# Kernel optimization log

Hardware: AMD Instinct MI355X
Metric: run time of the kernel (lower is better)

The kernel has to match this reference:

```python
import jax, jax.numpy as jnp
import numpy as np

NUM_HEADS = 12
SEQ_H = 32
SEQ_W = 32
D_HALF = 32
ROPE_BASE = 10000.0
LN_EPS = 1e-5


def build_rope_cache(seq_len, head_dim, base=ROPE_BASE):
    inv_freq = 1.0 / base ** (jnp.arange(0, head_dim, 2, dtype=jnp.float32) / head_dim)
    t = jnp.arange(seq_len, dtype=jnp.float32)
    freqs = jnp.outer(t, inv_freq)  # [seq_len, head_dim//2]
    cos = jnp.repeat(jnp.cos(freqs), 2, axis=-1)  # [seq_len, head_dim]
    sin = jnp.repeat(jnp.sin(freqs), 2, axis=-1)
    return cos, sin


def apply_rope(x, cos, sin):
    # x: [B,H,N,d_sub], cos/sin: [N,d_sub]
    x_even, x_odd = x[..., ::2], x[..., 1::2]
    x_rot = jnp.stack([-x_odd, x_even], axis=-1).reshape(x.shape)
    return x * cos[None, None] + x_rot * sin[None, None]


def setup_inputs() -> dict:
    key = jax.random.key(0)
    ks = jax.random.split(key, 3)
    B, N, D = 8, 1025, 768
    return {
        "x": jax.random.normal(ks[0], (B, N, D), dtype=jnp.float32),
        "ln_g": jnp.ones((D,), dtype=jnp.float32),
        "ln_b": jnp.zeros((D,), dtype=jnp.float32),
        "w_qkv": jax.random.normal(ks[1], (3 * D, D), dtype=jnp.float32) * 0.02,
        "w_proj": jax.random.normal(ks[2], (D, D), dtype=jnp.float32) * 0.02,
        "b_proj": jnp.zeros((D,), dtype=jnp.float32),
    }


def reference(x, ln_g, ln_b, w_qkv, w_proj, b_proj):
    B, N, D = x.shape
    H = NUM_HEADS
    hd = D // H
    d2 = D_HALF
    scale = hd ** -0.5

    # LayerNorm
    mu = jnp.mean(x, axis=-1, keepdims=True)
    var = jnp.mean(jnp.square(x - mu), axis=-1, keepdims=True)
    xn = (x - mu) * jax.lax.rsqrt(var + LN_EPS) * ln_g + ln_b

    # QKV projection (no bias)
    qkv = jnp.einsum("bnd,ed->bne", xn, w_qkv).reshape(B, N, 3, H, hd)
    qkv = jnp.transpose(qkv, (2, 0, 3, 1, 4))  # [3,B,H,N,hd]
    q, k, v = qkv[0], qkv[1], qkv[2]

    # 2D position ids (CLS token -> row 0, col 0)
    patch_lin = jnp.arange(N - 1)
    rows = patch_lin // SEQ_W
    cols = patch_lin % SEQ_W
    zero = jnp.zeros((1,), dtype=patch_lin.dtype)
    row_ids = jnp.concatenate([zero, rows])
    col_ids = jnp.concatenate([zero, cols])

    cos_row, sin_row = build_rope_cache(SEQ_H, d2)
    cos_col, sin_col = build_rope_cache(SEQ_W, d2)
    cos_r, sin_r = cos_row[row_ids], sin_row[row_ids]  # [N,d2]
    cos_c, sin_c = cos_col[col_ids], sin_col[col_ids]

    q = jnp.concatenate(
        [apply_rope(q[..., :d2], cos_r, sin_r), apply_rope(q[..., d2:], cos_c, sin_c)], axis=-1)
    k = jnp.concatenate(
        [apply_rope(k[..., :d2], cos_r, sin_r), apply_rope(k[..., d2:], cos_c, sin_c)], axis=-1)

    attn = jnp.einsum("bhqd,bhkd->bhqk", q, k) * scale
    attn = jax.nn.softmax(attn, axis=-1)
    out = jnp.einsum("bhqk,bhkd->bhqd", attn, v)  # [B,H,N,hd]
    out = jnp.transpose(out, (0, 2, 1, 3)).reshape(B, N, D)
    return jnp.einsum("bnd,ed->bne", out, w_proj) + b_proj
```

## Files before the change

kernel.cpp:

```cpp
#include <hip/hip_runtime.h>
#include <hip/hip_bf16.h>

typedef unsigned short u16;

#define B_      8
#define N_      1025
#define D_      768
#define H_      12
#define HD_     64
#define M_REAL  (B_ * N_)
#define M_PAD   8320
#define QKVC    (3 * D_)
#define LN_BLK  (M_REAL / 4)

typedef __attribute__((ext_vector_type(8))) short bf16x8;
typedef __attribute__((ext_vector_type(4))) float f32x4;

static __device__ __forceinline__ float bf2f(u16 u) {
    union { unsigned int i; float f; } v; v.i = ((unsigned int)u) << 16; return v.f;
}
static __device__ __forceinline__ u16 f2bf(float f) {
    union { float f; unsigned int i; } v; v.f = f;
    unsigned int x = v.i;
    return (u16)((x + 0x7fffu + ((x >> 16) & 1u)) >> 16);
}
static __device__ __forceinline__ unsigned int cvtpk(float a, float b) {
    unsigned int r;
    asm volatile("v_cvt_pk_bf16_f32 %0, %1, %2" : "=v"(r) : "v"(a), "v"(b));
    return r;
}

static __device__ __forceinline__ void g2l16(const u16* g, u16* l) {
    __builtin_amdgcn_global_load_lds(
        (const __attribute__((address_space(1))) unsigned int*)g,
        (__attribute__((address_space(3))) unsigned int*)l, 16, 0, 0);
}

__global__ __launch_bounds__(256)
void ln_f2b_kernel(const float* __restrict__ x, const float* __restrict__ g,
                   const float* __restrict__ bvec, u16* __restrict__ xn,
                   const float* __restrict__ wq, u16* __restrict__ wqb,
                   const float* __restrict__ wp, u16* __restrict__ wpb)
{
    const int tid = threadIdx.x;
    if (blockIdx.x >= LN_BLK) {
        int i = (blockIdx.x - LN_BLK) * 1024 + tid * 4;
        const float* src; u16* dst;
        if (i < QKVC * D_) { src = wq + i; dst = wqb + i; }
        else { src = wp + (i - QKVC * D_); dst = wpb + (i - QKVC * D_); }
        float4 v = *(const float4*)src;
        dst[0] = f2bf(v.x); dst[1] = f2bf(v.y);
        dst[2] = f2bf(v.z); dst[3] = f2bf(v.w);
        return;
    }
    const int wave = tid >> 6, lane = tid & 63;
    const int row  = blockIdx.x * 4 + wave;
    const float* xr = x + (size_t)row * D_;
    float4 v[3];
    float s = 0.f, ss = 0.f;
#pragma unroll
    for (int j = 0; j < 3; j++) {
        float4 t = *(const float4*)&xr[j * 256 + lane * 4];
        v[j] = t;
        s  += (t.x + t.y) + (t.z + t.w);
        ss += (t.x * t.x + t.y * t.y) + (t.z * t.z + t.w * t.w);
    }
#pragma unroll
    for (int off = 1; off < 64; off <<= 1) {
        s  += __shfl_xor(s,  off);
        ss += __shfl_xor(ss, off);
    }
    const float mean = s * (1.0f / D_);
    const float var  = ss * (1.0f / D_) - mean * mean;
    const float rs   = rsqrtf(var + 1e-5f);
    u16* outr = xn + (size_t)row * D_;
#pragma unroll
    for (int j = 0; j < 3; j++) {
        int c = j * 256 + lane * 4;
        float4 g4 = *(const float4*)&g[c];
        float4 b4 = *(const float4*)&bvec[c];
        u16 o[4];
        o[0] = f2bf((v[j].x - mean) * rs * g4.x + b4.x);
        o[1] = f2bf((v[j].y - mean) * rs * g4.y + b4.y);
        o[2] = f2bf((v[j].z - mean) * rs * g4.z + b4.z);
        o[3] = f2bf((v[j].w - mean) * rs * g4.w + b4.w);
        *(uint2*)&outr[c] = *(const uint2*)o;
    }
}

template <typename OutT, bool ROPE>
__global__ __launch_bounds__(256)
void gemm_bt(const u16* __restrict__ A, const u16* __restrict__ B,
             OutT* __restrict__ C, const float* __restrict__ bias,
             int M_real, int Ncols, int K,
             int BM, int BN, int gh, int gw, int PC)
{
    const int l   = blockIdx.x;
    const int xcd = l & 7;
    const int i0  = l >> 3;
    const int pr  = xcd / PC, pc = xcd % PC;
    const int bm  = pr * gh + (i0 % gh);
    const int bn  = pc * gw + (i0 / gh);
    if (bm >= BM || bn >= BN) return;

    __shared__ __align__(16) unsigned char smem[34816];
    u16* As0 = (u16*)smem;
    u16* Bs0 = (u16*)(smem + 8192);
    u16*   ep16 = (u16*)smem;
    float* ep32 = (float*)smem;

    const int tid  = threadIdx.x;
    const int wave = tid >> 6, lane = tid & 63;
    const int wm   = (wave >> 1) * 64, wn = (wave & 1) * 64;
    const int lrow = lane & 15, lq = lane >> 4;
    const int lrow4 = lane >> 2, lchunk = lane & 3;

    int ar0 = bm * 128 + wave * 16 + lrow4;       if (ar0 >= M_real) ar0 = M_real - 1;
    int ar1 = bm * 128 + (wave + 4) * 16 + lrow4; if (ar1 >= M_real) ar1 = M_real - 1;
    const u16* apg0 = A + (size_t)ar0 * K + lchunk * 8;
    const u16* apg1 = A + (size_t)ar1 * K + lchunk * 8;
    const u16* bpg0 = B + (size_t)(bn * 128 + wave * 16 + lrow4) * K + lchunk * 8;
    const u16* bpg1 = B + (size_t)(bn * 128 + (wave + 4) * 16 + lrow4) * K + lchunk * 8;
    u16* asl0 = As0 + wave * 512;       u16* asl1 = As0 + (wave + 4) * 512;
    u16* bsl0 = Bs0 + wave * 512;       u16* bsl1 = Bs0 + (wave + 4) * 512;
    const int bufoff = 8192;

    f32x4 acc[4][4];
#pragma unroll
    for (int i = 0; i < 4; i++)
#pragma unroll
        for (int j = 0; j < 4; j++)
            acc[i][j] = (f32x4){0.f, 0.f, 0.f, 0.f};

    g2l16(apg0, asl0); g2l16(apg1, asl1);
    g2l16(bpg0, bsl0); g2l16(bpg1, bsl1);

    const int kTiles = K / 32;
    for (int kt = 0; kt < kTiles; kt++) {
        const int cur = kt & 1;
        if (kt + 1 < kTiles) {
            const int k1 = (kt + 1) * 32;
            const int no = (cur ^ 1) * bufoff;
            g2l16(apg0 + k1, asl0 + no); g2l16(apg1 + k1, asl1 + no);
            g2l16(bpg0 + k1, bsl0 + no); g2l16(bpg1 + k1, bsl1 + no);
            asm volatile("s_waitcnt vmcnt(4)" ::: "memory");
        } else {
            asm volatile("s_waitcnt vmcnt(0)" ::: "memory");
        }
        __builtin_amdgcn_s_barrier();

        const u16* Asr = As0 + cur * bufoff;
        const u16* Bsr = Bs0 + cur * bufoff;
        bf16x8 af[4], bfr[4];
#pragma unroll
        for (int i = 0; i < 4; i++) {
            af[i]  = *(const bf16x8*)&Asr[(wm + i * 16 + lrow) * 32 + lq * 8];
            bfr[i] = *(const bf16x8*)&Bsr[(wn + i * 16 + lrow) * 32 + lq * 8];
        }
        __builtin_amdgcn_s_setprio(1);
#pragma unroll
        for (int i = 0; i < 4; i++)
#pragma unroll
            for (int j = 0; j < 4; j++)
                acc[i][j] = __builtin_amdgcn_mfma_f32_16x16x32_bf16(af[i], bfr[j], acc[i][j], 0, 0, 0);
        __builtin_amdgcn_s_setprio(0);
        __builtin_amdgcn_s_barrier();
    }
    __syncthreads();

    if constexpr (sizeof(OutT) == 2) {
#pragma unroll
        for (int j = 0; j < 4; j++) {
            int gcol = bn * 128 + wn + j * 16 + lrow;
            float bv = bias ? bias[gcol] : 0.f;
            int qk = gcol / D_;
            int dh = gcol & 63;
            int half = dh >> 5, ii = (dh & 31) >> 1;
            float sgn = (dh & 1) ? 1.f : -1.f;
            float invf = exp2f(-(float)ii * 0.8304820237218406f);
#pragma unroll
            for (int i = 0; i < 4; i++)
#pragma unroll
                for (int r = 0; r < 4; r++) {
                    int grow = bm * 128 + wm + i * 16 + lq * 4 + r;
                    float val = acc[i][j][r] + bv;
                    if constexpr (ROPE) {
                        if (qk < 2) {
                            float partner = __shfl_xor(val, 1);
                            int n = grow % N_;
                            int pl = n - 1;
                            int pos = (n == 0) ? 0 : (half ? (pl & 31) : (pl >> 5));
                            float ang = (float)pos * invf;
                            val = val * __cosf(ang) + sgn * partner * __sinf(ang);
                            if (qk == 0) val *= 0.125f;
                        }
                    }
                    ep16[(wm + i * 16 + lq * 4 + r) * 136 + wn + j * 16 + lrow] = f2bf(val);
                }
        }
        __syncthreads();
#pragma unroll
        for (int c = 0; c < 8; c++) {
            int idx = tid + c * 256;
            int row = idx >> 4, l16 = idx & 15;
            int grow = bm * 128 + row;
            if (grow < M_real)
                *(uint4*)((u16*)C + (size_t)grow * Ncols + bn * 128 + l16 * 8) =
                    *(const uint4*)&ep16[row * 136 + l16 * 8];
        }
    } else {
#pragma unroll
        for (int s = 0; s < 2; s++) {
            if (s) __syncthreads();
            if (wm == s * 64) {
#pragma unroll
                for (int j = 0; j < 4; j++) {
                    int gcol = bn * 128 + wn + j * 16 + lrow;
                    float bv = bias ? bias[gcol] : 0.f;
#pragma unroll
                    for (int i = 0; i < 4; i++)
#pragma unroll
                        for (int r = 0; r < 4; r++)
                            ep32[(i * 16 + lq * 4 + r) * 132 + wn + j * 16 + lrow] =
                                acc[i][j][r] + bv;
                }
            }
            __syncthreads();
#pragma unroll
            for (int c = 0; c < 8; c++) {
                int idx = tid + c * 256;
                int row = idx >> 5, l32 = idx & 31;
                int grow = bm * 128 + s * 64 + row;
                if (grow < M_real)
                    *(uint4*)((float*)C + (size_t)grow * Ncols + bn * 128 + l32 * 4) =
                        *(const uint4*)&ep32[row * 132 + l32 * 4];
            }
        }
    }
}

__global__ __launch_bounds__(256)
void attn_mfma(const u16* __restrict__ qkv, u16* __restrict__ out)
{
    __shared__ __align__(16) u16 Kt[2][64][64];
    __shared__ __align__(16) u16 Vt[2][64][64];

    const int l   = blockIdx.x;
    const int xcd = l & 7;
    const int j0  = l >> 3;
    const int bh  = xcd * 12 + j0 / 5;
    const int b  = bh / H_, h = bh % H_;
    const int q0 = (j0 % 5) * 256;
    const int tid  = threadIdx.x;
    const int wave = tid >> 6, lane = tid & 63;
    const int lm = lane & 15, lq = lane >> 4;
    const int qw = q0 + wave * 64;

    const int vcol = (lane & 35) | ((lane & 12) << 1) | ((lane & 16) >> 2);

    bf16x8 qf[4][2];
#pragma unroll
    for (int sq = 0; sq < 4; sq++) {
        int qrow = qw + sq * 16 + lm; if (qrow > N_ - 1) qrow = N_ - 1;
        const u16* qptr = qkv + (size_t)(b * N_ + qrow) * QKVC + h * HD_;
        qf[sq][0] = *(const bf16x8*)(qptr + lq * 8);
        qf[sq][1] = *(const bf16x8*)(qptr + 32 + lq * 8);
    }

    float l_r[4] = {0.f, 0.f, 0.f, 0.f};
    f32x4 o_acc[4][4];
#pragma unroll
    for (int sq = 0; sq < 4; sq++)
#pragma unroll
        for (int t = 0; t < 4; t++)
            o_acc[sq][t] = (f32x4){0.f, 0.f, 0.f, 0.f};

    bf16x8 kreg[2], vreg[2];
    {
        int krow = lane; if (krow > N_ - 1) krow = N_ - 1;
        const u16* kvp = qkv + (size_t)(b * N_ + krow) * QKVC + h * HD_;
#pragma unroll
        for (int p = 0; p < 2; p++) {
            int dg = wave + p * 4;
            kreg[p] = *(const bf16x8*)(kvp + D_ + dg * 8);
            vreg[p] = *(const bf16x8*)(kvp + 2 * D_ + dg * 8);
        }
    }

    const int kTiles = (N_ + 63) / 64;
    for (int kt = 0; kt < kTiles; kt++) {
        const int kbase = kt * 64;
        const int buf = kt & 1;

#pragma unroll
        for (int pp = 0; pp < 2; pp++) {
            int dg = wave + pp * 4;
            *(bf16x8*)&Kt[buf][lane][(dg ^ (lane & 7)) * 8] = kreg[pp];
#pragma unroll
            for (int j = 0; j < 8; j++)
                Vt[buf][dg * 8 + j][vcol ^ (j << 3)] = (u16)vreg[pp][j];
        }

        if (kt + 1 < kTiles) {
            int krow = kbase + 64 + lane; if (krow > N_ - 1) krow = N_ - 1;
            const u16* kvp = qkv + (size_t)(b * N_ + krow) * QKVC + h * HD_;
#pragma unroll
            for (int pp = 0; pp < 2; pp++) {
                int dg = wave + pp * 4;
                kreg[pp] = *(const bf16x8*)(kvp + D_ + dg * 8);
                vreg[pp] = *(const bf16x8*)(kvp + 2 * D_ + dg * 8);
            }
        }

        asm volatile("s_waitcnt lgkmcnt(0)" ::: "memory");
        __builtin_amdgcn_s_barrier();

        f32x4 sc[4][4];
        __builtin_amdgcn_s_setprio(1);
#pragma unroll
        for (int st = 0; st < 4; st++) {
            const int krow = st * 16 + lm;
            const int c0 = lq ^ (krow & 7);
            bf16x8 kf0 = *(const bf16x8*)&Kt[buf][krow][c0 * 8];
            bf16x8 kf1 = *(const bf16x8*)&Kt[buf][krow][(c0 ^ 4) * 8];
#pragma unroll
            for (int sq = 0; sq < 4; sq++) {
                f32x4 s4 = (f32x4){0.f, 0.f, 0.f, 0.f};
                s4 = __builtin_amdgcn_mfma_f32_16x16x32_bf16(kf0, qf[sq][0], s4, 0, 0, 0);
                s4 = __builtin_amdgcn_mfma_f32_16x16x32_bf16(kf1, qf[sq][1], s4, 0, 0, 0);
                sc[sq][st] = s4;
            }
        }
        __builtin_amdgcn_s_setprio(0);

        const bool lastT = (kt == kTiles - 1);
        bf16x8 pa[4][2];
#pragma unroll
        for (int sq = 0; sq < 4; sq++) {
            union { bf16x8 v; unsigned int u[4]; } pk0, pk1;
#pragma unroll
            for (int st = 0; st < 4; st++) {
                float p0 = __expf(sc[sq][st][0]);
                float p1 = __expf(sc[sq][st][1]);
                float p2 = __expf(sc[sq][st][2]);
                float p3 = __expf(sc[sq][st][3]);
                if (lastT) {
                    const int keyb = kbase + st * 16 + lq * 4;
                    if (keyb + 0 >= N_) p0 = 0.f;
                    if (keyb + 1 >= N_) p1 = 0.f;
                    if (keyb + 2 >= N_) p2 = 0.f;
                    if (keyb + 3 >= N_) p3 = 0.f;
                }
                l_r[sq] += (p0 + p1) + (p2 + p3);
                unsigned int lo = cvtpk(p0, p1);
                unsigned int hi = cvtpk(p2, p3);
                if      (st == 0) { pk0.u[0] = lo; pk0.u[1] = hi; }
                else if (st == 1) { pk0.u[2] = lo; pk0.u[3] = hi; }
                else if (st == 2) { pk1.u[0] = lo; pk1.u[1] = hi; }
                else              { pk1.u[2] = lo; pk1.u[3] = hi; }
            }
            pa[sq][0] = pk0.v; pa[sq][1] = pk1.v;
        }

        __builtin_amdgcn_s_setprio(1);
#pragma unroll
        for (int nt = 0; nt < 4; nt++) {
            const int vrow = nt * 16 + lm;
            const int d0 = lq ^ (vrow & 7);
            bf16x8 vb0 = *(const bf16x8*)&Vt[buf][vrow][d0 * 8];
            bf16x8 vb1 = *(const bf16x8*)&Vt[buf][vrow][(d0 ^ 4) * 8];
#pragma unroll
            for (int sq = 0; sq < 4; sq++) {
                o_acc[sq][nt] = __builtin_amdgcn_mfma_f32_16x16x32_bf16(pa[sq][0], vb0, o_acc[sq][nt], 0, 0, 0);
                o_acc[sq][nt] = __builtin_amdgcn_mfma_f32_16x16x32_bf16(pa[sq][1], vb1, o_acc[sq][nt], 0, 0, 0);
            }
        }
        __builtin_amdgcn_s_setprio(0);
    }

    float lfull[4];
#pragma unroll
    for (int sq = 0; sq < 4; sq++) {
        float l2 = l_r[sq];
        l2 += __shfl_xor(l2, 16);
        l2 += __shfl_xor(l2, 32);
        lfull[sq] = l2;
    }

#pragma unroll
    for (int sq = 0; sq < 4; sq++)
#pragma unroll
        for (int r = 0; r < 4; r++) {
            int q = qw + sq * 16 + lq * 4 + r;
            if (q < N_) {
                float inv = 1.0f / __shfl(lfull[sq], lq * 4 + r);
                u16* orow = out + (size_t)(b * N_ + q) * D_ + h * HD_ + lm;
#pragma unroll
                for (int nt = 0; nt < 4; nt++)
                    orow[nt * 16] = f2bf(o_acc[sq][nt][r] * inv);
            }
        }
}

extern "C" void kernel_launch(void* const* d_in, const int* in_sizes, int n_in,
                              void* d_out, int out_size, void* d_ws, size_t ws_size,
                              hipStream_t stream)
{
    const float* x      = (const float*)d_in[0];
    const float* ln_g   = (const float*)d_in[1];
    const float* ln_b   = (const float*)d_in[2];
    const float* w_qkv  = (const float*)d_in[3];
    const float* w_proj = (const float*)d_in[4];
    const float* b_proj = (const float*)d_in[5];

    u16* wqkv_b  = (u16*)d_ws;
    u16* wproj_b = wqkv_b + (size_t)QKVC * D_;
    u16* xn      = wproj_b + (size_t)D_ * D_;
    u16* qkv     = xn + (size_t)M_PAD * D_;
    u16* attno   = xn;

    ln_f2b_kernel<<<LN_BLK + (QKVC * D_ + D_ * D_) / 1024, 256, 0, stream>>>(
        x, ln_g, ln_b, xn, w_qkv, wqkv_b, w_proj, wproj_b);

    gemm_bt<u16, true><<<1224, 256, 0, stream>>>(
        xn, wqkv_b, qkv, nullptr, M_REAL, QKVC, D_,
        65, 18, 17, 9, 2);

    attn_mfma<<<480, 256, 0, stream>>>(qkv, attno);

    gemm_bt<float, false><<<432, 256, 0, stream>>>(
        attno, wproj_b, (float*)d_out, b_proj, M_REAL, D_, D_,
        65, 6, 9, 6, 1);
}
```

Before: 208.1 us.

## Enlarge GEMM block tile to 256x128 with 128x64 per-wave tiles

Both GEMMs now use 256-row by 128-column block tiles instead of 128x128. Each wave computes 8x4 MFMA tiles, and A fragments are loaded inside the loop. The change aims to reuse each loaded B tile across more rows and cut block count and global traffic per FLOP. In exchange it raises accumulator registers and LDS use (48KB), which may lower occupancy, and grid counts drop (648 and 240 blocks), which can underfill the CUs, especially for the output projection. The epilogues are reworked into staged passes to fit the larger tile.

New measurement: 293.2 us. 40.9% more time.

```diff
diff --git a/kernel.cpp b/kernel.cpp
--- a/kernel.cpp
+++ b/kernel.cpp
@@ -103,37 +103,45 @@
     const int bn  = pc * gw + (i0 / gh);
     if (bm >= BM || bn >= BN) return;
 
-    __shared__ __align__(16) unsigned char smem[34816];
+    __shared__ __align__(16) unsigned char smem[49152];
     u16* As0 = (u16*)smem;
-    u16* Bs0 = (u16*)(smem + 8192);
+    u16* Bs0 = (u16*)(smem + 16384);
     u16*   ep16 = (u16*)smem;
     float* ep32 = (float*)smem;
+    const int bufoff = 12288;
 
     const int tid  = threadIdx.x;
     const int wave = tid >> 6, lane = tid & 63;
-    const int wm   = (wave >> 1) * 64, wn = (wave & 1) * 64;
+    const int wr   = wave >> 1, wc = wave & 1;
     const int lrow = lane & 15, lq = lane >> 4;
     const int lrow4 = lane >> 2, lchunk = lane & 3;
 
-    int ar0 = bm * 128 + wave * 16 + lrow4;       if (ar0 >= M_real) ar0 = M_real - 1;
-    int ar1 = bm * 128 + (wave + 4) * 16 + lrow4; if (ar1 >= M_real) ar1 = M_real - 1;
-    const u16* apg0 = A + (size_t)ar0 * K + lchunk * 8;
-    const u16* apg1 = A + (size_t)ar1 * K + lchunk * 8;
-    const u16* bpg0 = B + (size_t)(bn * 128 + wave * 16 + lrow4) * K + lchunk * 8;
-    const u16* bpg1 = B + (size_t)(bn * 128 + (wave + 4) * 16 + lrow4) * K + lchunk * 8;
-    u16* asl0 = As0 + wave * 512;       u16* asl1 = As0 + (wave + 4) * 512;
-    u16* bsl0 = Bs0 + wave * 512;       u16* bsl1 = Bs0 + (wave + 4) * 512;
-    const int bufoff = 8192;
-
-    f32x4 acc[4][4];
-#pragma unroll
-    for (int i = 0; i < 4; i++)
+    const u16* apg[4]; u16* asl[4];
+    const u16* bpg[2]; u16* bsl[2];
+#pragma unroll
+    for (int t = 0; t < 4; t++) {
+        int ar = bm * 256 + wave * 16 + t * 64 + lrow4;
+        if (ar >= M_real) ar = M_real - 1;
+        apg[t] = A + (size_t)ar * K + lchunk * 8;
+        asl[t] = As0 + (wave * 16 + t * 64) * 32;
+    }
+#pragma unroll
+    for (int t = 0; t < 2; t++) {
+        bpg[t] = B + (size_t)(bn * 128 + wave * 16 + t * 64 + lrow4) * K + lchunk * 8;
+        bsl[t] = Bs0 + (wave * 16 + t * 64) * 32;
+    }
+
+    f32x4 acc[8][4];
+#pragma unroll
+    for (int i = 0; i < 8; i++)
 #pragma unroll
         for (int j = 0; j < 4; j++)
             acc[i][j] = (f32x4){0.f, 0.f, 0.f, 0.f};
 
-    g2l16(apg0, asl0); g2l16(apg1, asl1);
-    g2l16(bpg0, bsl0); g2l16(bpg1, bsl1);
+#pragma unroll
+    for (int t = 0; t < 4; t++) g2l16(apg[t], asl[t]);
+#pragma unroll
+    for (int t = 0; t < 2; t++) g2l16(bpg[t], bsl[t]);
 
     const int kTiles = K / 32;
     for (int kt = 0; kt < kTiles; kt++) {
@@ -141,9 +149,11 @@
         if (kt + 1 < kTiles) {
             const int k1 = (kt + 1) * 32;
             const int no = (cur ^ 1) * bufoff;
-            g2l16(apg0 + k1, asl0 + no); g2l16(apg1 + k1, asl1 + no);
-            g2l16(bpg0 + k1, bsl0 + no); g2l16(bpg1 + k1, bsl1 + no);
-            asm volatile("s_waitcnt vmcnt(4)" ::: "memory");
+#pragma unroll
+            for (int t = 0; t < 4; t++) g2l16(apg[t] + k1, asl[t] + no);
+#pragma unroll
+            for (int t = 0; t < 2; t++) g2l16(bpg[t] + k1, bsl[t] + no);
+            asm volatile("s_waitcnt vmcnt(6)" ::: "memory");
         } else {
             asm volatile("s_waitcnt vmcnt(0)" ::: "memory");
         }
@@ -151,18 +161,18 @@
 
         const u16* Asr = As0 + cur * bufoff;
         const u16* Bsr = Bs0 + cur * bufoff;
-        bf16x8 af[4], bfr[4];
-#pragma unroll
-        for (int i = 0; i < 4; i++) {
-            af[i]  = *(const bf16x8*)&Asr[(wm + i * 16 + lrow) * 32 + lq * 8];
-            bfr[i] = *(const bf16x8*)&Bsr[(wn + i * 16 + lrow) * 32 + lq * 8];
-        }
+        bf16x8 bfr[4];
+#pragma unroll
+        for (int j = 0; j < 4; j++)
+            bfr[j] = *(const bf16x8*)&Bsr[(wc * 64 + j * 16 + lrow) * 32 + lq * 8];
         __builtin_amdgcn_s_setprio(1);
 #pragma unroll
-        for (int i = 0; i < 4; i++)
+        for (int i = 0; i < 8; i++) {
+            bf16x8 af = *(const bf16x8*)&Asr[(wr * 128 + i * 16 + lrow) * 32 + lq * 8];
 #pragma unroll
             for (int j = 0; j < 4; j++)
-                acc[i][j] = __builtin_amdgcn_mfma_f32_16x16x32_bf16(af[i], bfr[j], acc[i][j], 0, 0, 0);
+                acc[i][j] = __builtin_amdgcn_mfma_f32_16x16x32_bf16(af, bfr[j], acc[i][j], 0, 0, 0);
+        }
         __builtin_amdgcn_s_setprio(0);
         __builtin_amdgcn_s_barrier();
     }
@@ -170,59 +180,66 @@
 
     if constexpr (sizeof(OutT) == 2) {
 #pragma unroll
-        for (int j = 0; j < 4; j++) {
-            int gcol = bn * 128 + wn + j * 16 + lrow;
-            float bv = bias ? bias[gcol] : 0.f;
-            int qk = gcol / D_;
-            int dh = gcol & 63;
-            int half = dh >> 5, ii = (dh & 31) >> 1;
-            float sgn = (dh & 1) ? 1.f : -1.f;
-            float invf = exp2f(-(float)ii * 0.8304820237218406f);
-#pragma unroll
-            for (int i = 0; i < 4; i++)
-#pragma unroll
-                for (int r = 0; r < 4; r++) {
-                    int grow = bm * 128 + wm + i * 16 + lq * 4 + r;
-                    float val = acc[i][j][r] + bv;
-                    if constexpr (ROPE) {
-                        if (qk < 2) {
-                            float partner = __shfl_xor(val, 1);
-                            int n = grow % N_;
-                            int pl = n - 1;
-                            int pos = (n == 0) ? 0 : (half ? (pl & 31) : (pl >> 5));
-                            float ang = (float)pos * invf;
-                            val = val * __cosf(ang) + sgn * partner * __sinf(ang);
-                            if (qk == 0) val *= 0.125f;
-                        }
-                    }
-                    ep16[(wm + i * 16 + lq * 4 + r) * 136 + wn + j * 16 + lrow] = f2bf(val);
-                }
-        }
-        __syncthreads();
-#pragma unroll
-        for (int c = 0; c < 8; c++) {
-            int idx = tid + c * 256;
-            int row = idx >> 4, l16 = idx & 15;
-            int grow = bm * 128 + row;
-            if (grow < M_real)
-                *(uint4*)((u16*)C + (size_t)grow * Ncols + bn * 128 + l16 * 8) =
-                    *(const uint4*)&ep16[row * 136 + l16 * 8];
-        }
-    } else {
-#pragma unroll
         for (int s = 0; s < 2; s++) {
             if (s) __syncthreads();
-            if (wm == s * 64) {
+            if (wr == s) {
 #pragma unroll
                 for (int j = 0; j < 4; j++) {
-                    int gcol = bn * 128 + wn + j * 16 + lrow;
+                    int gcol = bn * 128 + wc * 64 + j * 16 + lrow;
                     float bv = bias ? bias[gcol] : 0.f;
+                    int qk = gcol / D_;
+                    int dh = gcol & 63;
+                    int half = dh >> 5, ii = (dh & 31) >> 1;
+                    float sgn = (dh & 1) ? 1.f : -1.f;
+                    float invf = exp2f(-(float)ii * 0.8304820237218406f);
+#pragma unroll
+                    for (int i = 0; i < 8; i++)
+#pragma unroll
+                        for (int r = 0; r < 4; r++) {
+                            int grow = bm * 256 + s * 128 + i * 16 + lq * 4 + r;
+                            float val = acc[i][j][r] + bv;
+                            if constexpr (ROPE) {
+                                if (qk < 2) {
+                                    float partner = __shfl_xor(val, 1);
+                                    int n = grow % N_;
+                                    int pl = n - 1;
+                                    int pos = (n == 0) ? 0 : (half ? (pl & 31) : (pl >> 5));
+                                    float ang = (float)pos * invf;
+                                    val = val * __cosf(ang) + sgn * partner * __sinf(ang);
+                                    if (qk == 0) val *= 0.125f;
+                                }
+                            }
+                            ep16[(i * 16 + lq * 4 + r) * 136 + wc * 64 + j * 16 + lrow] = f2bf(val);
+                        }
+                }
+            }
+            __syncthreads();
+#pragma unroll
+            for (int c = 0; c < 8; c++) {
+                int idx = tid + c * 256;
+                int row = idx >> 4, l16 = idx & 15;
+                int grow = bm * 256 + s * 128 + row;
+                if (grow < M_real)
+                    *(uint4*)((u16*)C + (size_t)grow * Ncols + bn * 128 + l16 * 8) =
+                        *(const uint4*)&ep16[row * 136 + l16 * 8];
+            }
+        }
+    } else {
+#pragma unroll
+        for (int s = 0; s < 4; s++) {
+            if (s) __syncthreads();
+            if (wr == (s >> 1)) {
+                const int io = (s & 1) * 4;
+#pragma unroll
+                for (int j = 0; j < 4; j++) {
+                    int gcol = bn * 128 + wc * 64 + j * 16 + lrow;
+                    float bv = bias ? bias[gcol] : 0.f;
 #pragma unroll
                     for (int i = 0; i < 4; i++)
 #pragma unroll
                         for (int r = 0; r < 4; r++)
-                            ep32[(i * 16 + lq * 4 + r) * 132 + wn + j * 16 + lrow] =
-                                acc[i][j][r] + bv;
+                            ep32[(i * 16 + lq * 4 + r) * 132 + wc * 64 + j * 16 + lrow] =
+                                acc[io + i][j][r] + bv;
                 }
             }
             __syncthreads();
@@ -230,7 +247,7 @@
             for (int c = 0; c < 8; c++) {
                 int idx = tid + c * 256;
                 int row = idx >> 5, l32 = idx & 31;
-                int grow = bm * 128 + s * 64 + row;
+                int grow = bm * 256 + s * 64 + row;
                 if (grow < M_real)
                     *(uint4*)((float*)C + (size_t)grow * Ncols + bn * 128 + l32 * 4) =
                         *(const uint4*)&ep32[row * 132 + l32 * 4];
@@ -422,13 +439,13 @@
     ln_f2b_kernel<<<LN_BLK + (QKVC * D_ + D_ * D_) / 1024, 256, 0, stream>>>(
         x, ln_g, ln_b, xn, w_qkv, wqkv_b, w_proj, wproj_b);
 
-    gemm_bt<u16, true><<<1224, 256, 0, stream>>>(
+    gemm_bt<u16, true><<<648, 256, 0, stream>>>(
         xn, wqkv_b, qkv, nullptr, M_REAL, QKVC, D_,
-        65, 18, 17, 9, 2);
+        33, 18, 9, 9, 2);
 
     attn_mfma<<<480, 256, 0, stream>>>(qkv, attno);
 
-    gemm_bt<float, false><<<432, 256, 0, stream>>>(
+    gemm_bt<float, false><<<240, 256, 0, stream>>>(
         attno, wproj_b, (float*)d_out, b_proj, M_REAL, D_, D_,
-        65, 6, 9, 6, 1);
-}
+        33, 6, 5, 6, 1);
+}
```

## Load GEMM A operand directly from global into registers, bypassing LDS

Applied to the files above, without the earlier changes.

The GEMM main loop now keeps only the B tile in shared memory. Each wave loads its A fragments straight from global memory into registers, double-buffered across two unrolled k-steps. This removes the A-side LDS writes and reads and halves LDS traffic. The cost is that A rows are fetched redundantly by the two waves sharing the same rows, with less coalesced 16-byte loads, more registers, and vmcnt wait counts that must stay correct.

Result: slower. 257.0 us (+23.5%).

```diff
diff --git a/kernel.cpp b/kernel.cpp
--- a/kernel.cpp
+++ b/kernel.cpp
@@ -104,10 +104,10 @@
     if (bm >= BM || bn >= BN) return;
 
     __shared__ __align__(16) unsigned char smem[34816];
-    u16* As0 = (u16*)smem;
-    u16* Bs0 = (u16*)(smem + 8192);
+    u16* Bs0 = (u16*)smem;
     u16*   ep16 = (u16*)smem;
     float* ep32 = (float*)smem;
+    const int bufoffB = 4096;
 
     const int tid  = threadIdx.x;
     const int wave = tid >> 6, lane = tid & 63;
@@ -115,15 +115,18 @@
     const int lrow = lane & 15, lq = lane >> 4;
     const int lrow4 = lane >> 2, lchunk = lane & 3;
 
-    int ar0 = bm * 128 + wave * 16 + lrow4;       if (ar0 >= M_real) ar0 = M_real - 1;
-    int ar1 = bm * 128 + (wave + 4) * 16 + lrow4; if (ar1 >= M_real) ar1 = M_real - 1;
-    const u16* apg0 = A + (size_t)ar0 * K + lchunk * 8;
-    const u16* apg1 = A + (size_t)ar1 * K + lchunk * 8;
     const u16* bpg0 = B + (size_t)(bn * 128 + wave * 16 + lrow4) * K + lchunk * 8;
     const u16* bpg1 = B + (size_t)(bn * 128 + (wave + 4) * 16 + lrow4) * K + lchunk * 8;
-    u16* asl0 = As0 + wave * 512;       u16* asl1 = As0 + (wave + 4) * 512;
-    u16* bsl0 = Bs0 + wave * 512;       u16* bsl1 = Bs0 + (wave + 4) * 512;
-    const int bufoff = 8192;
+    u16* bsl0 = Bs0 + wave * 512;
+    u16* bsl1 = Bs0 + (wave + 4) * 512;
+
+    const u16* apg[4];
+#pragma unroll
+    for (int i = 0; i < 4; i++) {
+        int ar = bm * 128 + wm + i * 16 + lrow;
+        if (ar >= M_real) ar = M_real - 1;
+        apg[i] = A + (size_t)ar * K + lq * 8;
+    }
 
     f32x4 acc[4][4];
 #pragma unroll
@@ -132,39 +135,63 @@
         for (int j = 0; j < 4; j++)
             acc[i][j] = (f32x4){0.f, 0.f, 0.f, 0.f};
 
-    g2l16(apg0, asl0); g2l16(apg1, asl1);
+    bf16x8 a0[4], a1[4];
     g2l16(bpg0, bsl0); g2l16(bpg1, bsl1);
+#pragma unroll
+    for (int i = 0; i < 4; i++) a0[i] = *(const bf16x8*)apg[i];
 
     const int kTiles = K / 32;
-    for (int kt = 0; kt < kTiles; kt++) {
-        const int cur = kt & 1;
+    for (int kt = 0; kt < kTiles; kt += 2) {
         if (kt + 1 < kTiles) {
             const int k1 = (kt + 1) * 32;
-            const int no = (cur ^ 1) * bufoff;
-            g2l16(apg0 + k1, asl0 + no); g2l16(apg1 + k1, asl1 + no);
-            g2l16(bpg0 + k1, bsl0 + no); g2l16(bpg1 + k1, bsl1 + no);
-            asm volatile("s_waitcnt vmcnt(4)" ::: "memory");
+            g2l16(bpg0 + k1, bsl0 + bufoffB); g2l16(bpg1 + k1, bsl1 + bufoffB);
+#pragma unroll
+            for (int i = 0; i < 4; i++) a1[i] = *(const bf16x8*)(apg[i] + k1);
+            asm volatile("s_waitcnt vmcnt(6)" ::: "memory");
         } else {
             asm volatile("s_waitcnt vmcnt(0)" ::: "memory");
         }
         __builtin_amdgcn_s_barrier();
-
-        const u16* Asr = As0 + cur * bufoff;
-        const u16* Bsr = Bs0 + cur * bufoff;
-        bf16x8 af[4], bfr[4];
-#pragma unroll
-        for (int i = 0; i < 4; i++) {
-            af[i]  = *(const bf16x8*)&Asr[(wm + i * 16 + lrow) * 32 + lq * 8];
-            bfr[i] = *(const bf16x8*)&Bsr[(wn + i * 16 + lrow) * 32 + lq * 8];
-        }
-        __builtin_amdgcn_s_setprio(1);
-#pragma unroll
-        for (int i = 0; i < 4; i++)
+        {
+            const u16* Bsr = Bs0;
+            bf16x8 bfr[4];
 #pragma unroll
             for (int j = 0; j < 4; j++)
-                acc[i][j] = __builtin_amdgcn_mfma_f32_16x16x32_bf16(af[i], bfr[j], acc[i][j], 0, 0, 0);
-        __builtin_amdgcn_s_setprio(0);
-        __builtin_amdgcn_s_barrier();
+                bfr[j] = *(const bf16x8*)&Bsr[(wn + j * 16 + lrow) * 32 + lq * 8];
+            __builtin_amdgcn_s_setprio(1);
+#pragma unroll
+            for (int i = 0; i < 4; i++)
+#pragma unroll
+                for (int j = 0; j < 4; j++)
+                    acc[i][j] = __builtin_amdgcn_mfma_f32_16x16x32_bf16(a0[i], bfr[j], acc[i][j], 0, 0, 0);
+            __builtin_amdgcn_s_setprio(0);
+            __builtin_amdgcn_s_barrier();
+        }
+        if (kt + 1 < kTiles) {
+            if (kt + 2 < kTiles) {
+                const int k2 = (kt + 2) * 32;
+                g2l16(bpg0 + k2, bsl0); g2l16(bpg1 + k2, bsl1);
+#pragma unroll
+                for (int i = 0; i < 4; i++) a0[i] = *(const bf16x8*)(apg[i] + k2);
+                asm volatile("s_waitcnt vmcnt(6)" ::: "memory");
+            } else {
+                asm volatile("s_waitcnt vmcnt(0)" ::: "memory");
+            }
+            __builtin_amdgcn_s_barrier();
+            const u16* Bsr = Bs0 + bufoffB;
+            bf16x8 bfr[4];
+#pragma unroll
+            for (int j = 0; j < 4; j++)
+                bfr[j] = *(const bf16x8*)&Bsr[(wn + j * 16 + lrow) * 32 + lq * 8];
+            __builtin_amdgcn_s_setprio(1);
+#pragma unroll
+            for (int i = 0; i < 4; i++)
+#pragma unroll
+                for (int j = 0; j < 4; j++)
+                    acc[i][j] = __builtin_amdgcn_mfma_f32_16x16x32_bf16(a1[i], bfr[j], acc[i][j], 0, 0, 0);
+            __builtin_amdgcn_s_setprio(0);
+            __builtin_amdgcn_s_barrier();
+        }
     }
     __syncthreads();
 
```
